# Performance work log

Hardware: AMD Instinct MI355X
Metric: run time of the kernel (lower is better)

## Reference

```python
import jax, jax.numpy as jnp
import numpy as np

B, N, L = 512, 64, 64
D = 256          # item_embed_size / hidden_size
H = 256          # linear_hidden_size
V = 100000       # item_size
STEP = 1


def _p(key, shape, std=0.0625):
    return jax.random.uniform(key, shape, jnp.float32, -std, std)


def setup_inputs() -> dict:
    key = jax.random.key(0)
    ks = jax.random.split(key, 32)
    inp = {
        "alias_inputs": jax.random.randint(ks[0], (B, L), 0, N),
        "A": jax.random.uniform(ks[1], (B, N, 2 * N), jnp.float32),
        "items": jax.random.randint(ks[2], (B, N), 0, V),
        "mask": jnp.ones((B, L), jnp.int32),
        # parameters (stored as [in, out]; torch Linear applies x @ W.T + b)
        "emb": _p(ks[3], (V, D)),
        "W_ein": _p(ks[4], (D, D)), "b_ein": _p(ks[5], (D,)),
        "W_eout": _p(ks[6], (D, D)), "b_eout": _p(ks[7], (D,)),
        "b_iah": _p(ks[8], (D,)), "b_oah": _p(ks[9], (D,)),
        "W_i": _p(ks[10], (2 * D, 3 * D)), "b_i": _p(ks[11], (3 * D,)),
        "W_h": _p(ks[12], (D, 3 * D)), "b_h": _p(ks[13], (3 * D,)),
        "W1": _p(ks[14], (D, D)), "b1": _p(ks[15], (D,)),
        "W2": _p(ks[16], (D, D)), "b2": _p(ks[17], (D,)),
        "W3": _p(ks[18], (D, 1)),
        "Wn1": _p(ks[19], (2 * D, H)), "bn1": _p(ks[20], (H,)),
        "Wn2": _p(ks[21], (H, D)), "bn2": _p(ks[22], (D,)),
    }
    return inp


def reference(alias_inputs, A, items, mask,
              emb, W_ein, b_ein, W_eout, b_eout, b_iah, b_oah,
              W_i, b_i, W_h, b_h, W1, b1, W2, b2, W3, Wn1, bn1, Wn2, bn2):
    n = A.shape[1]
    hidden = emb[items]  # [B, N, D] (dropout is identity at eval)

    def gnn_cell(h):
        inp_in = jnp.matmul(A[:, :, :n], h @ W_ein + b_ein) + b_iah
        inp_out = jnp.matmul(A[:, :, n:2 * n], h @ W_eout + b_eout) + b_oah
        inputs = jnp.concatenate([inp_in, inp_out], axis=2)     # [B, N, 2D]
        gi = inputs @ W_i + b_i                                  # [B, N, 3D]
        gh = h @ W_h + b_h                                       # [B, N, 3D]
        i_r, i_i, i_n = jnp.split(gi, 3, axis=2)
        h_r, h_i, h_n = jnp.split(gh, 3, axis=2)
        resetgate = jax.nn.sigmoid(i_r + h_r)
        inputgate = jax.nn.sigmoid(i_i + h_i)
        newgate = jnp.tanh(i_n + resetgate * h_n)
        return newgate + inputgate * (h - newgate)

    for _ in range(STEP):
        hidden = gnn_cell(hidden)

    # per-sample gather of node states into sequence order
    seq_hidden = jnp.take_along_axis(hidden, alias_inputs[:, :, None], axis=1)  # [B, L, D]
    last = jnp.sum(mask, axis=1) - 1
    ht = seq_hidden[jnp.arange(seq_hidden.shape[0]), last]        # [B, D]

    q1 = (ht @ W1 + b1)[:, None, :]                               # [B, 1, D]
    q2 = seq_hidden @ W2 + b2                                     # [B, L, D]
    alpha = jax.nn.sigmoid(q1 + q2) @ W3                          # [B, L, 1]
    a = jnp.sum(alpha * seq_hidden * mask[:, :, None].astype(jnp.float32), axis=1)  # [B, D]

    x = jnp.concatenate([a, ht], axis=1)                          # [B, 2D]
    return jax.nn.relu(x @ Wn1 + bn1) @ Wn2 + bn2                 # [B, D]
```

## Files before the change

kernel.cpp:

```cpp
#include <hip/hip_runtime.h>
#include <hip/hip_bf16.h>
#include <math.h>

typedef short bhalf8 __attribute__((ext_vector_type(8)));
typedef float floatx4 __attribute__((ext_vector_type(4)));

__device__ __forceinline__ float sigmoidf_(float x) { return 1.0f / (1.0f + __expf(-x)); }

__device__ __forceinline__ unsigned short f2bf(float f) {
    unsigned int u = __builtin_bit_cast(unsigned int, f);
    u += 0x7FFFu + ((u >> 16) & 1u);
    return (unsigned short)(u >> 16);
}
__device__ __forceinline__ float bf2f(unsigned short h) {
    unsigned int u = ((unsigned int)h) << 16;
    return __builtin_bit_cast(float, u);
}

__device__ __forceinline__ floatx4 mfma16(bhalf8 a, bhalf8 b, floatx4 c) {
    return __builtin_amdgcn_mfma_f32_16x16x32_bf16(a, b, c, 0, 0, 0);
}

__device__ __forceinline__ void gl_lds16(const unsigned short* g, unsigned short* l) {
    __builtin_amdgcn_global_load_lds(
        (const __attribute__((address_space(1))) void*)g,
        (__attribute__((address_space(3))) void*)l, 16, 0, 0);
}

__device__ __forceinline__ void pack_generic(
    int b, int tid, const float* __restrict__ W0, const float* __restrict__ W1,
    int split, int N, int BN, unsigned short* __restrict__ out)
{
    int t = b * 256 + tid;
    int j = t & 7;
    int lane = (t >> 3) & 63;
    int FT = BN >> 4;
    int f = (t >> 9) % FT;
    int rest = t / (512 * FT);
    int NT = N / BN;
    int nt = rest % NT;
    int kt = rest / NT;
    int k = kt * 32 + (lane >> 4) * 8 + j;
    int n = nt * BN + f * 16 + (lane & 15);
    float v = (n < split) ? W0[(size_t)k * split + n]
                          : W1[(size_t)k * (N - split) + (n - split)];
    out[t] = f2bf(v);
}

__device__ __forceinline__ void pack_gru_(
    int b, int tid, const float* __restrict__ Wi, const float* __restrict__ Wh,
    unsigned short* __restrict__ out)
{
    int t = b * 256 + tid;
    int j = t & 7;
    int lane = (t >> 3) & 63;
    int f = (t >> 9) & 3;
    int q = t >> 11;
    int g = q % 3;
    int p = q / 3;
    int dt = p & 3;
    int kt = p >> 2;
    int k = kt * 32 + (lane >> 4) * 8 + j;
    int n = g * 256 + dt * 64 + f * 16 + (lane & 15);
    float v = (k < 512) ? Wi[(size_t)k * 768 + n] : Wh[(size_t)(k - 512) * 768 + n];
    out[t] = f2bf(v);
}

__global__ __launch_bounds__(256) void pack_all(
    const float* __restrict__ W_ein, const float* __restrict__ W_eout,
    const float* __restrict__ Wi, const float* __restrict__ Wh,
    const float* __restrict__ W2, const float* __restrict__ Wn1,
    const float* __restrict__ Wn2,
    unsigned short* __restrict__ Wio_pk, unsigned short* __restrict__ Wg_pk,
    unsigned short* __restrict__ W2pk, unsigned short* __restrict__ Wn1pk,
    unsigned short* __restrict__ Wn2pk)
{
    int bx = blockIdx.x;
    int tid = threadIdx.x;
    if (bx < 512)       pack_generic(bx,        tid, W_ein, W_eout, 256, 512, 128, Wio_pk);
    else if (bx < 2816) pack_gru_   (bx - 512,  tid, Wi, Wh, Wg_pk);
    else if (bx < 3072) pack_generic(bx - 2816, tid, W2,  W2,  256, 256, 256, W2pk);
    else if (bx < 3584) pack_generic(bx - 3072, tid, Wn1, Wn1, 256, 256, 256, Wn1pk);
    else                pack_generic(bx - 3584, tid, Wn2, Wn2, 256, 256, 256, Wn2pk);
}

__global__ __launch_bounds__(256) void gather_emb(
    const int* __restrict__ items, const float* __restrict__ emb,
    unsigned short* __restrict__ hidden_pk)
{
    int i = blockIdx.x * 256 + threadIdx.x;
    int mg = i >> 9;
    int rem = i & 511;
    int l = rem & 63;
    int m = mg * 16 + (l & 15);
    int k = (rem >> 6) * 32 + (l >> 4) * 8;
    int it = items[m];
    const float* src = emb + (size_t)it * 256 + k;
    float4 v0 = *(const float4*)src;
    float4 v1 = *(const float4*)(src + 4);
    uint4 o;
    o.x = f2bf(v0.x) | ((unsigned)f2bf(v0.y) << 16);
    o.y = f2bf(v0.z) | ((unsigned)f2bf(v0.w) << 16);
    o.z = f2bf(v1.x) | ((unsigned)f2bf(v1.y) << 16);
    o.w = f2bf(v1.z) | ((unsigned)f2bf(v1.w) << 16);
    *(uint4*)(hidden_pk + (size_t)i * 8) = o;
}

__global__ __launch_bounds__(256) void gemm_hio_mfma(
    const unsigned short* __restrict__ hidden_pk,
    const unsigned short* __restrict__ Wio_pk,
    const float* __restrict__ bein, const float* __restrict__ beout,
    unsigned short* __restrict__ hio_pk)
{
    __shared__ unsigned short As[2][4096];
    __shared__ unsigned short Bs[2][4096];
    const int tid = threadIdx.x;
    const int wid = tid >> 6, lane = tid & 63;
    const int wr = wid >> 1, wc = wid & 1;
    const int bm = blockIdx.x * 128;
    const int nt = blockIdx.y;
    const int mg0 = bm >> 4;

    auto stage = [&](int kt, int buf) {
        #pragma unroll
        for (int u = 0; u < 2; ++u) {
            int rg = wid * 2 + u;
            gl_lds16(hidden_pk + ((size_t)(mg0 + rg) * 8 + kt) * 512 + lane * 8, &As[buf][rg * 512]);
            gl_lds16(Wio_pk + ((size_t)(kt * 4 + nt) * 8 + rg) * 512 + lane * 8, &Bs[buf][rg * 512]);
        }
    };

    floatx4 acc[4][4] = {};
    stage(0, 0);
    __syncthreads();
    #pragma unroll
    for (int kt = 0; kt < 8; ++kt) {
        int cur = kt & 1;
        if (kt < 7) stage(kt + 1, cur ^ 1);
        bhalf8 a[4], b[4];
        #pragma unroll
        for (int i = 0; i < 4; i++) a[i] = *(const bhalf8*)&As[cur][(wr * 4 + i) * 512 + lane * 8];
        #pragma unroll
        for (int j = 0; j < 4; j++) b[j] = *(const bhalf8*)&Bs[cur][(wc * 4 + j) * 512 + lane * 8];
        #pragma unroll
        for (int i = 0; i < 4; i++)
            #pragma unroll
            for (int j = 0; j < 4; j++) acc[i][j] = mfma16(a[i], b[j], acc[i][j]);
        __syncthreads();
    }
    const int r0 = (lane >> 4) * 4;
    #pragma unroll
    for (int mf = 0; mf < 4; mf++) {
        int m0 = bm + wr * 64 + mf * 16 + r0;
        int b_ = m0 >> 6;
        int ml = m0 & 63;
        int ktb = ml >> 5;
        int k0 = ml & 31;
        int j0 = k0 & 7;
        #pragma unroll
        for (int nf = 0; nf < 4; nf++) {
            int ng = nt * 128 + wc * 64 + nf * 16 + (lane & 15);
            int half = ng >> 8;
            int nh = ng & 255;
            float bias = half ? beout[nh] : bein[nh];
            int lane_b = ((k0 >> 3) << 4) + (nh & 15);
            size_t pb = ((((size_t)(b_ * 2 + half) * 2 + ktb) * 16 + (nh >> 4)) * 64 + lane_b) * 8 + j0;
            ushort4 o;
            o.x = f2bf(acc[mf][nf][0] + bias);
            o.y = f2bf(acc[mf][nf][1] + bias);
            o.z = f2bf(acc[mf][nf][2] + bias);
            o.w = f2bf(acc[mf][nf][3] + bias);
            *(ushort4*)(hio_pk + pb) = o;
        }
    }
}

__global__ __launch_bounds__(256) void adj_mfma(
    const float* __restrict__ A,
    const unsigned short* __restrict__ hio_pk,
    const float* __restrict__ biah, const float* __restrict__ boah,
    unsigned short* __restrict__ inp_pk)
{
    __shared__ unsigned short As_[2048];
    __shared__ unsigned short Bs_[8192];
    const int b = blockIdx.x;
    const int half = blockIdx.y;
    const int tid = threadIdx.x;
    const int wid = tid >> 6, lane = tid & 63;

    floatx4 acc[4][4] = {};
    #pragma unroll
    for (int kt = 0; kt < 2; ++kt) {
        {
            int r = tid >> 2, jj = tid & 3;
            const float* src = A + (size_t)b * 8192 + r * 128 + half * 64 + kt * 32 + jj * 8;
            float4 v0 = *(const float4*)src;
            float4 v1 = *(const float4*)(src + 4);
            uint4 o;
            o.x = f2bf(v0.x) | ((unsigned)f2bf(v0.y) << 16);
            o.y = f2bf(v0.z) | ((unsigned)f2bf(v0.w) << 16);
            o.z = f2bf(v1.x) | ((unsigned)f2bf(v1.y) << 16);
            o.w = f2bf(v1.z) | ((unsigned)f2bf(v1.w) << 16);
            *(uint4*)&As_[((r >> 4) * 64 + jj * 16 + (r & 15)) * 8] = o;
        }
        {
            const unsigned short* src = hio_pk + (size_t)((b * 2 + half) * 2 + kt) * 8192;
            #pragma unroll
            for (int u = 0; u < 4; ++u) {
                int sg = wid * 4 + u;
                gl_lds16(src + sg * 512 + lane * 8, &Bs_[sg * 512]);
            }
        }
        __syncthreads();
        bhalf8 a[4], bb[4];
        #pragma unroll
        for (int i = 0; i < 4; i++) a[i] = *(const bhalf8*)&As_[(i * 64 + lane) * 8];
        #pragma unroll
        for (int j = 0; j < 4; j++) bb[j] = *(const bhalf8*)&Bs_[((wid * 4 + j) * 64 + lane) * 8];
        #pragma unroll
        for (int i = 0; i < 4; i++)
            #pragma unroll
            for (int j = 0; j < 4; j++) acc[i][j] = mfma16(a[i], bb[j], acc[i][j]);
        __syncthreads();
    }
    const float* bias = half ? boah : biah;
    const int r0 = (lane >> 4) * 4;
    #pragma unroll
    for (int i = 0; i < 4; i++) {
        #pragma unroll
        for (int j = 0; j < 4; j++) {
            int nh = wid * 64 + j * 16 + (lane & 15);
            float bv = bias[nh];
            int kt5 = half * 8 + wid * 2 + (j >> 1);
            int l2 = ((j & 1) * 2 + ((lane >> 3) & 1)) * 16;
            #pragma unroll
            for (int reg = 0; reg < 4; reg++) {
                int mlo = r0 + reg;
                size_t dst = (((size_t)(b * 4 + i) * 16 + kt5) * 64 + l2 + mlo) * 8 + (lane & 7);
                inp_pk[dst] = f2bf(acc[i][j][reg] + bv);
            }
        }
    }
}

__global__ __launch_bounds__(256) void gru_mfma(
    const unsigned short* __restrict__ inp_pk,
    const unsigned short* __restrict__ hidden_pk,
    const unsigned short* __restrict__ Wg_pk,
    const float* __restrict__ bi, const float* __restrict__ bh,
    unsigned short* __restrict__ newh_bf)
{
    __shared__ unsigned short As3[3][4096];
    __shared__ unsigned short Bs2[2][6144];
    const int tid = threadIdx.x;
    const int wid = tid >> 6, lane = tid & 63;
    const int bm = blockIdx.x * 128;
    const int dt = blockIdx.y;
    const int mg0 = bm >> 4;

    floatx4 R[2][4] = {}, I[2][4] = {}, N0[2][4] = {}, N1[2][4] = {};

    auto stageA = [&](int st, int buf) {
        #pragma unroll
        for (int u = 0; u < 2; ++u) {
            int rg = wid * 2 + u;
            const unsigned short* src = (st < 16)
                ? inp_pk    + ((size_t)(mg0 + rg) * 16 + st) * 512
                : hidden_pk + ((size_t)(mg0 + rg) * 8 + (st - 16)) * 512;
            gl_lds16(src + lane * 8, &As3[buf][rg * 512]);
        }
    };
    auto stageB = [&](int st, int buf) {
        #pragma unroll
        for (int u = 0; u < 3; ++u) {
            int sg = wid * 3 + u;
            gl_lds16(Wg_pk + ((size_t)(st * 4 + dt) * 12 + sg) * 512 + lane * 8,
                     &Bs2[buf][sg * 512]);
        }
    };

    stageA(0, 0);
    stageB(0, 0);
    stageA(1, 1);
    #pragma unroll
    for (int st = 0; st < 24; ++st) {
        const int ca = st % 3, cb = st & 1;
        if (st < 23) asm volatile("s_waitcnt vmcnt(2)" ::: "memory");
        else         asm volatile("s_waitcnt vmcnt(0)" ::: "memory");
        __builtin_amdgcn_s_barrier();
        __builtin_amdgcn_sched_barrier(0);
        if (st < 23) stageB(st + 1, cb ^ 1);
        if (st < 22) stageA(st + 2, (st + 2) % 3);
        bhalf8 a0 = *(const bhalf8*)&As3[ca][(wid * 2 + 0) * 512 + lane * 8];
        bhalf8 a1 = *(const bhalf8*)&As3[ca][(wid * 2 + 1) * 512 + lane * 8];
        #pragma unroll
        for (int j = 0; j < 4; ++j) {
            bhalf8 bv = *(const bhalf8*)&Bs2[cb][(0 * 4 + j) * 512 + lane * 8];
            R[0][j] = mfma16(a0, bv, R[0][j]);
            R[1][j] = mfma16(a1, bv, R[1][j]);
        }
        #pragma unroll
        for (int j = 0; j < 4; ++j) {
            bhalf8 bv = *(const bhalf8*)&Bs2[cb][(1 * 4 + j) * 512 + lane * 8];
            I[0][j] = mfma16(a0, bv, I[0][j]);
            I[1][j] = mfma16(a1, bv, I[1][j]);
        }
        if (st < 16) {
            #pragma unroll
            for (int j = 0; j < 4; ++j) {
                bhalf8 bv = *(const bhalf8*)&Bs2[cb][(2 * 4 + j) * 512 + lane * 8];
                N0[0][j] = mfma16(a0, bv, N0[0][j]);
                N0[1][j] = mfma16(a1, bv, N0[1][j]);
            }
        } else {
            #pragma unroll
            for (int j = 0; j < 4; ++j) {
                bhalf8 bv = *(const bhalf8*)&Bs2[cb][(2 * 4 + j) * 512 + lane * 8];
                N1[0][j] = mfma16(a0, bv, N1[0][j]);
                N1[1][j] = mfma16(a1, bv, N1[1][j]);
            }
        }
    }
    const int r0 = (lane >> 4) * 4;
    const int bd = dt * 64;
    #pragma unroll
    for (int i = 0; i < 2; i++) {
        #pragma unroll
        for (int j = 0; j < 4; j++) {
            int d = bd + j * 16 + (lane & 15);
            float bir = bi[d] + bh[d];
            float bii = bi[256 + d] + bh[256 + d];
            float bin = bi[512 + d];
            float bhn = bh[512 + d];
            #pragma unroll
            for (int reg = 0; reg < 4; reg++) {
                int m = bm + wid * 32 + i * 16 + r0 + reg;
                size_t hidx = (((size_t)(m >> 4) * 8 + (d >> 5)) * 64
                               + ((d >> 3) & 3) * 16 + (m & 15)) * 8 + (d & 7);
                float hv = bf2f(hidden_pk[hidx]);
                float rg = sigmoidf_(R[i][j][reg] + bir);
                float ig = sigmoidf_(I[i][j][reg] + bii);
                float ng = tanhf(N0[i][j][reg] + bin + rg * (N1[i][j][reg] + bhn));
                newh_bf[(size_t)m * 256 + d] = f2bf(ng + ig * (hv - ng));
            }
        }
    }
}

__global__ __launch_bounds__(256) void attn_fused(
    const unsigned short* __restrict__ newh_bf,
    const int* __restrict__ alias, const int* __restrict__ mask,
    const float* __restrict__ W1, const float* __restrict__ b1,
    const float* __restrict__ b2, const float* __restrict__ W3,
    const unsigned short* __restrict__ W2pk,
    unsigned short* __restrict__ ht_bf,
    unsigned short* __restrict__ a_bf)
{
    const int b = blockIdx.x;
    const int tid = threadIdx.x;
    const int wid = tid >> 6, lane = tid & 63;
    __shared__ int arow[64];
    __shared__ int node_s;
    __shared__ float hts[256];
    __shared__ float q1s[256];
    __shared__ float alphap[4][64];
    __shared__ float am[64];
    __shared__ unsigned short As[2048];
    __shared__ unsigned short Bs[8192];
    if (tid < 64) {
        arow[tid] = b * 64 + alias[b * 64 + tid];
        int mv = mask[b * 64 + tid];
        #pragma unroll
        for (int off = 32; off > 0; off >>= 1) mv += __shfl_xor(mv, off);
        if (tid == 0) node_s = b * 64 + alias[b * 64 + (mv - 1)];
    }
    __syncthreads();
    {
        unsigned short hv = newh_bf[(size_t)node_s * 256 + tid];
        ht_bf[(size_t)b * 256 + tid] = hv;
        hts[tid] = bf2f(hv);
    }
    __syncthreads();
    {
        float q0 = 0, q1v = 0, q2v = 0, q3v = 0;
        for (int k = 0; k < 256; k += 4) {
            q0  = fmaf(hts[k],     W1[(size_t)k * 256 + tid],       q0);
            q1v = fmaf(hts[k + 1], W1[(size_t)(k + 1) * 256 + tid], q1v);
            q2v = fmaf(hts[k + 2], W1[(size_t)(k + 2) * 256 + tid], q2v);
            q3v = fmaf(hts[k + 3], W1[(size_t)(k + 3) * 256 + tid], q3v);
        }
        q1s[tid] = (q0 + q1v) + (q2v + q3v) + b1[tid];
    }

    floatx4 acc[4][4] = {};
    #pragma unroll
    for (int kt = 0; kt < 8; ++kt) {
        {
            int r = tid >> 2, jj = tid & 3;
            const unsigned short* src = newh_bf + (size_t)arow[r] * 256 + kt * 32 + jj * 8;
            *(uint4*)&As[((r >> 4) * 64 + jj * 16 + (r & 15)) * 8] = *(const uint4*)src;
        }
        {
            const unsigned short* src = W2pk + (size_t)kt * 16 * 512;
            #pragma unroll
            for (int u = 0; u < 4; ++u) {
                int sg = wid * 4 + u;
                gl_lds16(src + sg * 512 + lane * 8, &Bs[sg * 512]);
            }
        }
        __syncthreads();
        bhalf8 a[4], bb[4];
        #pragma unroll
        for (int i = 0; i < 4; i++) a[i] = *(const bhalf8*)&As[(i * 64 + lane) * 8];
        #pragma unroll
        for (int j = 0; j < 4; j++) bb[j] = *(const bhalf8*)&Bs[((wid * 4 + j) * 64 + lane) * 8];
        #pragma unroll
        for (int i = 0; i < 4; i++)
            #pragma unroll
            for (int j = 0; j < 4; j++) acc[i][j] = mfma16(a[i], bb[j], acc[i][j]);
        __syncthreads();
    }
    float q1v[4], b2v[4], w3v[4];
    #pragma unroll
    for (int j = 0; j < 4; j++) {
        int col = wid * 64 + j * 16 + (lane & 15);
        q1v[j] = q1s[col];
        b2v[j] = b2[col];
        w3v[j] = W3[col];
    }
    #pragma unroll
    for (int i = 0; i < 4; i++) {
        #pragma unroll
        for (int reg = 0; reg < 4; reg++) {
            float t = 0.f;
            #pragma unroll
            for (int j = 0; j < 4; j++)
                t += sigmoidf_(acc[i][j][reg] + q1v[j] + b2v[j]) * w3v[j];
            #pragma unroll
            for (int off = 1; off < 16; off <<= 1) t += __shfl_xor(t, off);
            if ((lane & 15) == 0) alphap[wid][i * 16 + (lane >> 4) * 4 + reg] = t;
        }
    }
    __syncthreads();
    if (tid < 64) {
        float al = alphap[0][tid] + alphap[1][tid] + alphap[2][tid] + alphap[3][tid];
        am[tid] = al * (float)mask[b * 64 + tid];
    }
    __syncthreads();
    float acca = 0.f;
    #pragma unroll 8
    for (int l = 0; l < 64; ++l)
        acca = fmaf(am[l], bf2f(newh_bf[(size_t)arow[l] * 256 + tid]), acca);
    a_bf[(size_t)b * 256 + tid] = f2bf(acca);
}

__global__ __launch_bounds__(256) void mlp_fused(
    const unsigned short* __restrict__ a_bf, const unsigned short* __restrict__ ht_bf,
    const unsigned short* __restrict__ Wn1pk, const float* __restrict__ bn1,
    const unsigned short* __restrict__ Wn2pk, const float* __restrict__ bn2,
    float* __restrict__ out)
{
    __shared__ unsigned short As[2048];
    __shared__ unsigned short Bs[8192];
    __shared__ unsigned short Ys[16384];
    const int tid = threadIdx.x;
    const int wid = tid >> 6, lane = tid & 63;
    const int bm = blockIdx.x * 64;
    const int c = lane & 15;
    const int r0 = (lane >> 4) * 4;

    {
        floatx4 acc[4][4] = {};
        #pragma unroll
        for (int kt = 0; kt < 16; ++kt) {
            {
                int r = tid >> 2, jj = tid & 3;
                const unsigned short* src = ((kt < 8) ? a_bf : ht_bf)
                    + (size_t)(bm + r) * 256 + (kt & 7) * 32 + jj * 8;
                *(uint4*)&As[((r >> 4) * 64 + jj * 16 + (r & 15)) * 8] = *(const uint4*)src;
            }
            #pragma unroll
            for (int u = 0; u < 4; ++u) {
                int sg = wid * 4 + u;
                gl_lds16(Wn1pk + ((size_t)kt * 16 + sg) * 512 + lane * 8, &Bs[sg * 512]);
            }
            __syncthreads();
            bhalf8 a[4], bb[4];
            #pragma unroll
            for (int i = 0; i < 4; i++) a[i] = *(const bhalf8*)&As[(i * 64 + lane) * 8];
            #pragma unroll
            for (int j = 0; j < 4; j++) bb[j] = *(const bhalf8*)&Bs[((wid * 4 + j) * 64 + lane) * 8];
            #pragma unroll
            for (int i = 0; i < 4; i++)
                #pragma unroll
                for (int j = 0; j < 4; j++) acc[i][j] = mfma16(a[i], bb[j], acc[i][j]);
            __syncthreads();
        }
        #pragma unroll
        for (int i = 0; i < 4; i++) {
            #pragma unroll
            for (int jf = 0; jf < 4; jf++) {
                int n = wid * 64 + jf * 16 + c;
                float bv = bn1[n];
                int kt2 = wid * 2 + (jf >> 1);
                int l2 = ((jf & 1) * 2 + (c >> 3)) * 16;
                #pragma unroll
                for (int reg = 0; reg < 4; reg++) {
                    float v = fmaxf(acc[i][jf][reg] + bv, 0.f);
                    size_t idx = (((size_t)(kt2 * 4 + i) * 64) + l2 + r0 + reg) * 8 + (c & 7);
                    Ys[idx] = f2bf(v);
                }
            }
        }
    }
    __syncthreads();
    floatx4 acc2[4][4] = {};
    #pragma unroll
    for (int kt2 = 0; kt2 < 8; ++kt2) {
        #pragma unroll
        for (int u = 0; u < 4; ++u) {
            int sg = wid * 4 + u;
            gl_lds16(Wn2pk + ((size_t)kt2 * 16 + sg) * 512 + lane * 8, &Bs[sg * 512]);
        }
        __syncthreads();
        bhalf8 a[4], bb[4];
        #pragma unroll
        for (int i = 0; i < 4; i++) a[i] = *(const bhalf8*)&Ys[((kt2 * 4 + i) * 64 + lane) * 8];
        #pragma unroll
        for (int j = 0; j < 4; j++) bb[j] = *(const bhalf8*)&Bs[((wid * 4 + j) * 64 + lane) * 8];
        #pragma unroll
        for (int i = 0; i < 4; i++)
            #pragma unroll
            for (int j = 0; j < 4; j++) acc2[i][j] = mfma16(a[i], bb[j], acc2[i][j]);
        __syncthreads();
    }
    #pragma unroll
    for (int i = 0; i < 4; i++) {
        #pragma unroll
        for (int jf = 0; jf < 4; jf++) {
            int n = wid * 64 + jf * 16 + c;
            float bv = bn2[n];
            #pragma unroll
            for (int reg = 0; reg < 4; reg++) {
                int m = bm + i * 16 + r0 + reg;
                out[(size_t)m * 256 + n] = acc2[i][jf][reg] + bv;
            }
        }
    }
}

extern "C" void kernel_launch(void* const* d_in, const int* in_sizes, int n_in,
                              void* d_out, int out_size, void* d_ws, size_t ws_size,
                              hipStream_t stream)
{
    const int*   alias  = (const int*)  d_in[0];
    const float* A      = (const float*)d_in[1];
    const int*   items  = (const int*)  d_in[2];
    const int*   mask   = (const int*)  d_in[3];
    const float* emb    = (const float*)d_in[4];
    const float* W_ein  = (const float*)d_in[5];
    const float* b_ein  = (const float*)d_in[6];
    const float* W_eout = (const float*)d_in[7];
    const float* b_eout = (const float*)d_in[8];
    const float* b_iah  = (const float*)d_in[9];
    const float* b_oah  = (const float*)d_in[10];
    const float* W_i    = (const float*)d_in[11];
    const float* b_i    = (const float*)d_in[12];
    const float* W_h    = (const float*)d_in[13];
    const float* b_h    = (const float*)d_in[14];
    const float* W1     = (const float*)d_in[15];
    const float* b1     = (const float*)d_in[16];
    const float* W2     = (const float*)d_in[17];
    const float* b2     = (const float*)d_in[18];
    const float* W3     = (const float*)d_in[19];
    const float* Wn1    = (const float*)d_in[20];
    const float* bn1    = (const float*)d_in[21];
    const float* Wn2    = (const float*)d_in[22];
    const float* bn2    = (const float*)d_in[23];
    float* out = (float*)d_out;
    (void)in_sizes; (void)n_in; (void)out_size; (void)ws_size;

    char* w = (char*)d_ws;
    unsigned short* hidden_pk = (unsigned short*)(w);
    unsigned short* hio_pk    = (unsigned short*)(w + 16777216);
    unsigned short* inp_pk    = (unsigned short*)(w + 50331648);
    unsigned short* newh_bf   = (unsigned short*)(w + 83886080);
    unsigned short* Wio_pk    = (unsigned short*)(w + 100663296);
    unsigned short* Wg_pk     = (unsigned short*)(w + 100925440);
    unsigned short* W2pk      = (unsigned short*)(w + 102105088);
    unsigned short* Wn1pk     = (unsigned short*)(w + 102236160);
    unsigned short* Wn2pk     = (unsigned short*)(w + 102498304);
    unsigned short* ht_bf     = (unsigned short*)(w + 102629376);
    unsigned short* a_bf      = (unsigned short*)(w + 102891520);

    pack_all<<<3840, 256, 0, stream>>>(W_ein, W_eout, W_i, W_h, W2, Wn1, Wn2,
                                       Wio_pk, Wg_pk, W2pk, Wn1pk, Wn2pk);
    gather_emb   <<<4096, 256, 0, stream>>>(items, emb, hidden_pk);
    gemm_hio_mfma<<<dim3(256, 4), 256, 0, stream>>>(hidden_pk, Wio_pk, b_ein, b_eout, hio_pk);
    adj_mfma     <<<dim3(512, 2), 256, 0, stream>>>(A, hio_pk, b_iah, b_oah, inp_pk);
    gru_mfma     <<<dim3(256, 4), 256, 0, stream>>>(inp_pk, hidden_pk, Wg_pk, b_i, b_h, newh_bf);
    attn_fused   <<<512, 256, 0, stream>>>(newh_bf, alias, mask, W1, b1, b2, W3, W2pk, ht_bf, a_bf);
    mlp_fused    <<<8, 256, 0, stream>>>(a_bf, ht_bf, Wn1pk, bn1, Wn2pk, bn2, out);
}
```

Measured before the change: 167.9 us.

## Triple-buffer GEMM pipelines, move q1 to MFMA prep kernel, widen MLP K-steps

The hio GEMM and the GRU GEMM now use three LDS buffers, prefetching two stages ahead with explicit vmcnt waits and a single barrier per stage. The per-sample ht @ W1 projection, which was a scalar FMA loop inside every attention block, moves into a new 4-block MFMA kernel that also gathers ht and writes q1 to a global buffer. W1 is packed to bf16 alongside the other weights. The MLP kernel loads two K-tiles per barrier. In exchange this adds a kernel launch, uses more LDS (which may reduce occupancy), and rounds the W1 path to bf16.

```diff
diff --git a/kernel.cpp b/kernel.cpp
--- a/kernel.cpp
+++ b/kernel.cpp
@@ -70,10 +70,10 @@
     const float* __restrict__ W_ein, const float* __restrict__ W_eout,
     const float* __restrict__ Wi, const float* __restrict__ Wh,
     const float* __restrict__ W2, const float* __restrict__ Wn1,
-    const float* __restrict__ Wn2,
+    const float* __restrict__ Wn2, const float* __restrict__ W1,
     unsigned short* __restrict__ Wio_pk, unsigned short* __restrict__ Wg_pk,
     unsigned short* __restrict__ W2pk, unsigned short* __restrict__ Wn1pk,
-    unsigned short* __restrict__ Wn2pk)
+    unsigned short* __restrict__ Wn2pk, unsigned short* __restrict__ W1pk)
 {
     int bx = blockIdx.x;
     int tid = threadIdx.x;
@@ -81,7 +81,8 @@
     else if (bx < 2816) pack_gru_   (bx - 512,  tid, Wi, Wh, Wg_pk);
     else if (bx < 3072) pack_generic(bx - 2816, tid, W2,  W2,  256, 256, 256, W2pk);
     else if (bx < 3584) pack_generic(bx - 3072, tid, Wn1, Wn1, 256, 256, 256, Wn1pk);
-    else                pack_generic(bx - 3584, tid, Wn2, Wn2, 256, 256, 256, Wn2pk);
+    else if (bx < 3840) pack_generic(bx - 3584, tid, Wn2, Wn2, 256, 256, 256, Wn2pk);
+    else                pack_generic(bx - 3840, tid, W1,  W1,  256, 256, 256, W1pk);
 }
 
 __global__ __launch_bounds__(256) void gather_emb(
@@ -112,8 +113,8 @@
     const float* __restrict__ bein, const float* __restrict__ beout,
     unsigned short* __restrict__ hio_pk)
 {
-    __shared__ unsigned short As[2][4096];
-    __shared__ unsigned short Bs[2][4096];
+    __shared__ unsigned short As[3][4096];
+    __shared__ unsigned short Bs[3][4096];
     const int tid = threadIdx.x;
     const int wid = tid >> 6, lane = tid & 63;
     const int wr = wid >> 1, wc = wid & 1;
@@ -132,11 +133,15 @@
 
     floatx4 acc[4][4] = {};
     stage(0, 0);
-    __syncthreads();
+    stage(1, 1);
     #pragma unroll
     for (int kt = 0; kt < 8; ++kt) {
-        int cur = kt & 1;
-        if (kt < 7) stage(kt + 1, cur ^ 1);
+        const int cur = kt % 3;
+        if (kt < 7) asm volatile("s_waitcnt vmcnt(4)" ::: "memory");
+        else        asm volatile("s_waitcnt vmcnt(0)" ::: "memory");
+        __builtin_amdgcn_s_barrier();
+        __builtin_amdgcn_sched_barrier(0);
+        if (kt < 6) stage(kt + 2, (kt + 2) % 3);
         bhalf8 a[4], b[4];
         #pragma unroll
         for (int i = 0; i < 4; i++) a[i] = *(const bhalf8*)&As[cur][(wr * 4 + i) * 512 + lane * 8];
@@ -146,7 +151,6 @@
         for (int i = 0; i < 4; i++)
             #pragma unroll
             for (int j = 0; j < 4; j++) acc[i][j] = mfma16(a[i], b[j], acc[i][j]);
-        __syncthreads();
     }
     const int r0 = (lane >> 4) * 4;
     #pragma unroll
@@ -251,7 +255,7 @@
     unsigned short* __restrict__ newh_bf)
 {
     __shared__ unsigned short As3[3][4096];
-    __shared__ unsigned short Bs2[2][6144];
+    __shared__ unsigned short Bs3[3][6144];
     const int tid = threadIdx.x;
     const int wid = tid >> 6, lane = tid & 63;
     const int bm = blockIdx.x * 128;
@@ -275,47 +279,47 @@
         for (int u = 0; u < 3; ++u) {
             int sg = wid * 3 + u;
             gl_lds16(Wg_pk + ((size_t)(st * 4 + dt) * 12 + sg) * 512 + lane * 8,
-                     &Bs2[buf][sg * 512]);
+                     &Bs3[buf][sg * 512]);
         }
     };
 
     stageA(0, 0);
     stageB(0, 0);
     stageA(1, 1);
+    stageB(1, 1);
     #pragma unroll
     for (int st = 0; st < 24; ++st) {
-        const int ca = st % 3, cb = st & 1;
-        if (st < 23) asm volatile("s_waitcnt vmcnt(2)" ::: "memory");
+        const int ca = st % 3, cb = st % 3;
+        if (st < 23) asm volatile("s_waitcnt vmcnt(5)" ::: "memory");
         else         asm volatile("s_waitcnt vmcnt(0)" ::: "memory");
         __builtin_amdgcn_s_barrier();
         __builtin_amdgcn_sched_barrier(0);
-        if (st < 23) stageB(st + 1, cb ^ 1);
-        if (st < 22) stageA(st + 2, (st + 2) % 3);
+        if (st < 22) { stageA(st + 2, (st + 2) % 3); stageB(st + 2, (st + 2) % 3); }
         bhalf8 a0 = *(const bhalf8*)&As3[ca][(wid * 2 + 0) * 512 + lane * 8];
         bhalf8 a1 = *(const bhalf8*)&As3[ca][(wid * 2 + 1) * 512 + lane * 8];
         #pragma unroll
         for (int j = 0; j < 4; ++j) {
-            bhalf8 bv = *(const bhalf8*)&Bs2[cb][(0 * 4 + j) * 512 + lane * 8];
+            bhalf8 bv = *(const bhalf8*)&Bs3[cb][(0 * 4 + j) * 512 + lane * 8];
             R[0][j] = mfma16(a0, bv, R[0][j]);
             R[1][j] = mfma16(a1, bv, R[1][j]);
         }
         #pragma unroll
         for (int j = 0; j < 4; ++j) {
-            bhalf8 bv = *(const bhalf8*)&Bs2[cb][(1 * 4 + j) * 512 + lane * 8];
+            bhalf8 bv = *(const bhalf8*)&Bs3[cb][(1 * 4 + j) * 512 + lane * 8];
             I[0][j] = mfma16(a0, bv, I[0][j]);
             I[1][j] = mfma16(a1, bv, I[1][j]);
         }
         if (st < 16) {
             #pragma unroll
             for (int j = 0; j < 4; ++j) {
-                bhalf8 bv = *(const bhalf8*)&Bs2[cb][(2 * 4 + j) * 512 + lane * 8];
+                bhalf8 bv = *(const bhalf8*)&Bs3[cb][(2 * 4 + j) * 512 + lane * 8];
                 N0[0][j] = mfma16(a0, bv, N0[0][j]);
                 N0[1][j] = mfma16(a1, bv, N0[1][j]);
             }
         } else {
             #pragma unroll
             for (int j = 0; j < 4; ++j) {
-                bhalf8 bv = *(const bhalf8*)&Bs2[cb][(2 * 4 + j) * 512 + lane * 8];
+                bhalf8 bv = *(const bhalf8*)&Bs3[cb][(2 * 4 + j) * 512 + lane * 8];
                 N1[0][j] = mfma16(a0, bv, N1[0][j]);
                 N1[1][j] = mfma16(a1, bv, N1[1][j]);
             }
@@ -347,50 +351,88 @@
     }
 }
 
+__global__ __launch_bounds__(256) void prep_htq1(
+    const unsigned short* __restrict__ newh_bf,
+    const int* __restrict__ alias, const int* __restrict__ mask,
+    const unsigned short* __restrict__ W1pk, const float* __restrict__ b1,
+    unsigned short* __restrict__ ht_bf, float* __restrict__ q1buf)
+{
+    __shared__ unsigned short htile[32768];
+    __shared__ unsigned short Bs[8192];
+    const int tid = threadIdx.x;
+    const int wid = tid >> 6, lane = tid & 63;
+    const int bm = blockIdx.x * 128;
+
+    for (int it = 0; it < 32; ++it) {
+        int bb = bm + it * 4 + wid;
+        int mv = mask[bb * 64 + lane];
+        #pragma unroll
+        for (int off = 32; off > 0; off >>= 1) mv += __shfl_xor(mv, off);
+        int node = alias[bb * 64 + (mv - 1)];
+        size_t grow = (size_t)bb * 64 + node;
+        if (lane < 32) {
+            uint4 v = *(const uint4*)(newh_bf + grow * 256 + lane * 8);
+            *(uint4*)(ht_bf + (size_t)bb * 256 + lane * 8) = v;
+            int m = bb - bm;
+            int idx = (((lane >> 2) * 8 + (m >> 4)) * 64 + (lane & 3) * 16 + (m & 15)) * 8;
+            *(uint4*)&htile[idx] = v;
+        }
+    }
+    __syncthreads();
+
+    floatx4 acc[8][4] = {};
+    for (int kt = 0; kt < 8; ++kt) {
+        #pragma unroll
+        for (int u = 0; u < 4; ++u) {
+            int sg = wid * 4 + u;
+            gl_lds16(W1pk + ((size_t)kt * 16 + sg) * 512 + lane * 8, &Bs[sg * 512]);
+        }
+        __syncthreads();
+        bhalf8 a[8], bb[4];
+        #pragma unroll
+        for (int i = 0; i < 8; i++) a[i] = *(const bhalf8*)&htile[((kt * 8 + i) * 64 + lane) * 8];
+        #pragma unroll
+        for (int j = 0; j < 4; j++) bb[j] = *(const bhalf8*)&Bs[((wid * 4 + j) * 64 + lane) * 8];
+        #pragma unroll
+        for (int i = 0; i < 8; i++)
+            #pragma unroll
+            for (int j = 0; j < 4; j++) acc[i][j] = mfma16(a[i], bb[j], acc[i][j]);
+        __syncthreads();
+    }
+    const int r0 = (lane >> 4) * 4;
+    #pragma unroll
+    for (int i = 0; i < 8; i++) {
+        #pragma unroll
+        for (int j = 0; j < 4; j++) {
+            int col = wid * 64 + j * 16 + (lane & 15);
+            float bv = b1[col];
+            #pragma unroll
+            for (int reg = 0; reg < 4; reg++) {
+                int m = bm + i * 16 + r0 + reg;
+                q1buf[(size_t)m * 256 + col] = acc[i][j][reg] + bv;
+            }
+        }
+    }
+}
+
 __global__ __launch_bounds__(256) void attn_fused(
     const unsigned short* __restrict__ newh_bf,
     const int* __restrict__ alias, const int* __restrict__ mask,
-    const float* __restrict__ W1, const float* __restrict__ b1,
-    const float* __restrict__ b2, const float* __restrict__ W3,
+    const float* __restrict__ q1, const float* __restrict__ b2,
+    const float* __restrict__ W3,
     const unsigned short* __restrict__ W2pk,
-    unsigned short* __restrict__ ht_bf,
     unsigned short* __restrict__ a_bf)
 {
     const int b = blockIdx.x;
     const int tid = threadIdx.x;
     const int wid = tid >> 6, lane = tid & 63;
     __shared__ int arow[64];
-    __shared__ int node_s;
-    __shared__ float hts[256];
-    __shared__ float q1s[256];
     __shared__ float alphap[4][64];
     __shared__ float am[64];
     __shared__ unsigned short As[2048];
     __shared__ unsigned short Bs[8192];
-    if (tid < 64) {
-        arow[tid] = b * 64 + alias[b * 64 + tid];
-        int mv = mask[b * 64 + tid];
-        #pragma unroll
-        for (int off = 32; off > 0; off >>= 1) mv += __shfl_xor(mv, off);
-        if (tid == 0) node_s = b * 64 + alias[b * 64 + (mv - 1)];
-    }
+    if (tid < 64) arow[tid] = b * 64 + alias[b * 64 + tid];
     __syncthreads();
-    {
-        unsigned short hv = newh_bf[(size_t)node_s * 256 + tid];
-        ht_bf[(size_t)b * 256 + tid] = hv;
-        hts[tid] = bf2f(hv);
-    }
-    __syncthreads();
-    {
-        float q0 = 0, q1v = 0, q2v = 0, q3v = 0;
-        for (int k = 0; k < 256; k += 4) {
-            q0  = fmaf(hts[k],     W1[(size_t)k * 256 + tid],       q0);
-            q1v = fmaf(hts[k + 1], W1[(size_t)(k + 1) * 256 + tid], q1v);
-            q2v = fmaf(hts[k + 2], W1[(size_t)(k + 2) * 256 + tid], q2v);
-            q3v = fmaf(hts[k + 3], W1[(size_t)(k + 3) * 256 + tid], q3v);
-        }
-        q1s[tid] = (q0 + q1v) + (q2v + q3v) + b1[tid];
-    }
 
     floatx4 acc[4][4] = {};
     #pragma unroll
@@ -424,7 +466,7 @@
     #pragma unroll
     for (int j = 0; j < 4; j++) {
         int col = wid * 64 + j * 16 + (lane & 15);
-        q1v[j] = q1s[col];
+        q1v[j] = q1[(size_t)b * 256 + col];
         b2v[j] = b2[col];
         w3v[j] = W3[col];
     }
@@ -460,8 +502,8 @@
     const unsigned short* __restrict__ Wn2pk, const float* __restrict__ bn2,
     float* __restrict__ out)
 {
-    __shared__ unsigned short As[2048];
-    __shared__ unsigned short Bs[8192];
+    __shared__ unsigned short As[4096];
+    __shared__ unsigned short Bs[16384];
     __shared__ unsigned short Ys[16384];
     const int tid = threadIdx.x;
     const int wid = tid >> 6, lane = tid & 63;
@@ -472,28 +514,34 @@
     {
         floatx4 acc[4][4] = {};
         #pragma unroll
-        for (int kt = 0; kt < 16; ++kt) {
-            {
+        for (int s = 0; s < 8; ++s) {
+            #pragma unroll
+            for (int v = 0; v < 2; ++v) {
+                int kt = s * 2 + v;
                 int r = tid >> 2, jj = tid & 3;
                 const unsigned short* src = ((kt < 8) ? a_bf : ht_bf)
                     + (size_t)(bm + r) * 256 + (kt & 7) * 32 + jj * 8;
-                *(uint4*)&As[((r >> 4) * 64 + jj * 16 + (r & 15)) * 8] = *(const uint4*)src;
-            }
-            #pragma unroll
-            for (int u = 0; u < 4; ++u) {
-                int sg = wid * 4 + u;
-                gl_lds16(Wn1pk + ((size_t)kt * 16 + sg) * 512 + lane * 8, &Bs[sg * 512]);
+                *(uint4*)&As[v * 2048 + ((r >> 4) * 64 + jj * 16 + (r & 15)) * 8] = *(const uint4*)src;
+            }
+            #pragma unroll
+            for (int u = 0; u < 8; ++u) {
+                int sg = wid * 8 + u;
+                int ktl = sg >> 4, f = sg & 15;
+                gl_lds16(Wn1pk + ((size_t)(s * 2 + ktl) * 16 + f) * 512 + lane * 8, &Bs[sg * 512]);
             }
             __syncthreads();
-            bhalf8 a[4], bb[4];
-            #pragma unroll
-            for (int i = 0; i < 4; i++) a[i] = *(const bhalf8*)&As[(i * 64 + lane) * 8];
-            #pragma unroll
-            for (int j = 0; j < 4; j++) bb[j] = *(const bhalf8*)&Bs[((wid * 4 + j) * 64 + lane) * 8];
-            #pragma unroll
-            for (int i = 0; i < 4; i++)
+            #pragma unroll
+            for (int v = 0; v < 2; ++v) {
+                bhalf8 a[4], bb[4];
                 #pragma unroll
-                for (int j = 0; j < 4; j++) acc[i][j] = mfma16(a[i], bb[j], acc[i][j]);
+                for (int i = 0; i < 4; i++) a[i] = *(const bhalf8*)&As[v * 2048 + (i * 64 + lane) * 8];
+                #pragma unroll
+                for (int j = 0; j < 4; j++) bb[j] = *(const bhalf8*)&Bs[((v * 16) + wid * 4 + j) * 512 + lane * 8];
+                #pragma unroll
+                for (int i = 0; i < 4; i++)
+                    #pragma unroll
+                    for (int j = 0; j < 4; j++) acc[i][j] = mfma16(a[i], bb[j], acc[i][j]);
+            }
             __syncthreads();
         }
         #pragma unroll
@@ -516,22 +564,27 @@
     __syncthreads();
     floatx4 acc2[4][4] = {};
     #pragma unroll
-    for (int kt2 = 0; kt2 < 8; ++kt2) {
-        #pragma unroll
-        for (int u = 0; u < 4; ++u) {
-            int sg = wid * 4 + u;
-            gl_lds16(Wn2pk + ((size_t)kt2 * 16 + sg) * 512 + lane * 8, &Bs[sg * 512]);
-        }
-        __syncthreads();
-        bhalf8 a[4], bb[4];
-        #pragma unroll
-        for (int i = 0; i < 4; i++) a[i] = *(const bhalf8*)&Ys[((kt2 * 4 + i) * 64 + lane) * 8];
-        #pragma unroll
-        for (int j = 0; j < 4; j++) bb[j] = *(const bhalf8*)&Bs[((wid * 4 + j) * 64 + lane) * 8];
-        #pragma unroll
-        for (int i = 0; i < 4; i++)
-            #pragma unroll
-            for (int j = 0; j < 4; j++) acc2[i][j] = mfma16(a[i], bb[j], acc2[i][j]);
+    for (int s = 0; s < 4; ++s) {
+        #pragma unroll
+        for (int u = 0; u < 8; ++u) {
+            int sg = wid * 8 + u;
+            int ktl = sg >> 4, f = sg & 15;
+            gl_lds16(Wn2pk + ((size_t)(s * 2 + ktl) * 16 + f) * 512 + lane * 8, &Bs[sg * 512]);
+        }
+        __syncthreads();
+        #pragma unroll
+        for (int v = 0; v < 2; ++v) {
+            int kt2 = s * 2 + v;
+            bhalf8 a[4], bb[4];
+            #pragma unroll
+            for (int i = 0; i < 4; i++) a[i] = *(const bhalf8*)&Ys[((kt2 * 4 + i) * 64 + lane) * 8];
+            #pragma unroll
+            for (int j = 0; j < 4; j++) bb[j] = *(const bhalf8*)&Bs[((v * 16) + wid * 4 + j) * 512 + lane * 8];
+            #pragma unroll
+            for (int i = 0; i < 4; i++)
+                #pragma unroll
+                for (int j = 0; j < 4; j++) acc2[i][j] = mfma16(a[i], bb[j], acc2[i][j]);
+        }
         __syncthreads();
     }
     #pragma unroll
@@ -592,13 +645,16 @@
     unsigned short* Wn2pk     = (unsigned short*)(w + 102498304);
     unsigned short* ht_bf     = (unsigned short*)(w + 102629376);
     unsigned short* a_bf      = (unsigned short*)(w + 102891520);
-
-    pack_all<<<3840, 256, 0, stream>>>(W_ein, W_eout, W_i, W_h, W2, Wn1, Wn2,
-                                       Wio_pk, Wg_pk, W2pk, Wn1pk, Wn2pk);
+    unsigned short* W1pk      = (unsigned short*)(w + 103153664);
+    float*          q1buf     = (float*)         (w + 103284736);
+
+    pack_all<<<4096, 256, 0, stream>>>(W_ein, W_eout, W_i, W_h, W2, Wn1, Wn2, W1,
+                                       Wio_pk, Wg_pk, W2pk, Wn1pk, Wn2pk, W1pk);
     gather_emb   <<<4096, 256, 0, stream>>>(items, emb, hidden_pk);
     gemm_hio_mfma<<<dim3(256, 4), 256, 0, stream>>>(hidden_pk, Wio_pk, b_ein, b_eout, hio_pk);
     adj_mfma     <<<dim3(512, 2), 256, 0, stream>>>(A, hio_pk, b_iah, b_oah, inp_pk);
     gru_mfma     <<<dim3(256, 4), 256, 0, stream>>>(inp_pk, hidden_pk, Wg_pk, b_i, b_h, newh_bf);
-    attn_fused   <<<512, 256, 0, stream>>>(newh_bf, alias, mask, W1, b1, b2, W3, W2pk, ht_bf, a_bf);
+    prep_htq1    <<<4, 256, 0, stream>>>(newh_bf, alias, mask, W1pk, b1, ht_bf, q1buf);
+    attn_fused   <<<512, 256, 0, stream>>>(newh_bf, alias, mask, q1buf, b2, W3, W2pk, a_bf);
     mlp_fused    <<<8, 256, 0, stream>>>(a_bf, ht_bf, Wn1pk, bn1, Wn2pk, bn2, out);
 }
```

Result: slower. 196.3 us (+16.9%).
